# Kernel tuning notes

Measured on AMD Instinct MI355X. Metric: run time of the kernel, lower is better.

The kernel has to match this reference:

```python
import jax, jax.numpy as jnp
import numpy as np
from jax import lax

DN = ('NCHW', 'OIHW', 'NCHW')

def conv(x, w, b, stride, pad):
    y = lax.conv_general_dilated(x, w, (stride, stride), [(pad, pad), (pad, pad)], dimension_numbers=DN)
    return y + b[None, :, None, None]

def setup_inputs() -> dict:
    key = jax.random.key(0)
    ks = jax.random.split(key, 16)
    s = 0.05
    inp = {
        'condition': jax.random.normal(ks[0], (16, 1, 256, 256), jnp.float32),
        'w1': jax.random.normal(ks[1], (64, 1, 4, 4), jnp.float32) * s,
        'b1': jnp.zeros((64,), jnp.float32),
        'w2': jax.random.normal(ks[2], (128, 64, 4, 4), jnp.float32) * s,
        'b2': jnp.zeros((128,), jnp.float32),
        'w3': jax.random.normal(ks[3], (128, 128, 3, 3), jnp.float32) * s,
        'b3': jnp.zeros((128,), jnp.float32),
        'r1w1': jax.random.normal(ks[4], (32, 128, 3, 3), jnp.float32) * s,
        'r1b1': jnp.zeros((32,), jnp.float32),
        'r1w2': jax.random.normal(ks[5], (128, 32, 1, 1), jnp.float32) * s,
        'r1b2': jnp.zeros((128,), jnp.float32),
        'r2w1': jax.random.normal(ks[6], (32, 128, 3, 3), jnp.float32) * s,
        'r2b1': jnp.zeros((32,), jnp.float32),
        'r2w2': jax.random.normal(ks[7], (128, 32, 1, 1), jnp.float32) * s,
        'r2b2': jnp.zeros((128,), jnp.float32),
        'wpre': jax.random.normal(ks[8], (4, 128, 1, 1), jnp.float32) * s,
        'bpre': jnp.zeros((4,), jnp.float32),
        'codebook': jax.random.normal(ks[9], (2048, 4), jnp.float32),
    }
    return inp

def reference(condition, w1, b1, w2, b2, w3, b3, r1w1, r1b1, r1w2, r1b2,
              r2w1, r2b1, r2w2, r2b2, wpre, bpre, codebook):
    # --- conv encoder (VQ-VAE standard) ---
    h = jax.nn.relu(conv(condition, w1, b1, 2, 1))   # [B,64,128,128]
    h = jax.nn.relu(conv(h, w2, b2, 2, 1))           # [B,128,64,64]
    h = conv(h, w3, b3, 1, 1)                        # [B,128,64,64]
    # residual stack: 2 blocks of relu->3x3->relu->1x1, residual add
    for wa, ba, wb, bb in ((r1w1, r1b1, r1w2, r1b2), (r2w1, r2b1, r2w2, r2b2)):
        t = conv(jax.nn.relu(h), wa, ba, 1, 1)
        t = conv(jax.nn.relu(t), wb, bb, 1, 0)
        h = h + t
    h = jax.nn.relu(h)
    z = conv(h, wpre, bpre, 1, 0)                    # [B,4,64,64]
    # --- cosine-distance vector quantization ---
    B, D, H, W = z.shape
    zf = jnp.transpose(z, (0, 2, 3, 1)).reshape(-1, D)          # [BHW, D]
    zn = zf / (jnp.linalg.norm(zf, axis=-1, keepdims=True) + 1e-12)
    en = codebook / (jnp.linalg.norm(codebook, axis=-1, keepdims=True) + 1e-12)
    sim = jnp.einsum('nd,kd->nk', zn, en)                       # cosine similarity
    idx = jnp.argmax(sim, axis=-1)                              # nearest code
    q = codebook[idx].reshape(B, H, W, D)
    c = jnp.transpose(q, (0, 3, 1, 2))                          # [B,4,64,64]
    return c
```

## Files before the change

### kernel.cpp

```cpp
#include <hip/hip_runtime.h>
#include <math.h>


typedef short v8s __attribute__((ext_vector_type(8)));
typedef float v4f __attribute__((ext_vector_type(4)));

#define B_OFF 4194304
#define A_OFF 12582912
#define ENCB_F 1048576
#define ZB_F 2097152
#define W2_S 0
#define W3_S 393216
#define WR1_S 835584
#define WR2_S 946176
#define WP1_S 1056768
#define WP2_S 1069056

__device__ inline void limb3(float v, unsigned short& h, unsigned short& m,
                             unsigned short& l) {
    unsigned ub = __float_as_uint(v);
    unsigned hb = ub & 0xffff0000u;
    float r1 = v - __uint_as_float(hb);
    unsigned mb = __float_as_uint(r1) & 0xffff0000u;
    float r2 = r1 - __uint_as_float(mb);
    unsigned lb = __float_as_uint(r2) & 0xffff0000u;
    h = (unsigned short)(hb >> 16);
    m = (unsigned short)(mb >> 16);
    l = (unsigned short)(lb >> 16);
}

struct CfgConv2 {
    static constexpr int NC = 8, NT = 4, OC = 128;
    static constexpr bool RELU_IN = false, RELU_OUT = true;
    __device__ static void tap(int c, int t, int& ry, int& rx) {
        int py = (c >> 2) & 1, px = (c >> 1) & 1;
        ry = (t >> 1) - py; rx = (t & 1) - px;
    }
    __device__ static bool gaddr(int n, int oy, int r, int X, int icp, int c,
                                 int& g0, int& g1) {
        int py = (c >> 2) & 1, px = (c >> 1) & 1;
        int y2 = oy + r - 1;
        if (y2 < 0 || y2 >= 64) return false;
        int pi = (c & 1) * 16 + icp;
        g0 = (((n * 4 + py * 2 + px) * 64 + y2) * 32 + pi) * 128 + X;
        g1 = g0 + 64;
        return true;
    }
    __device__ static int widx(int c, int t, int oc, int ic) {
        int py = (c >> 2) & 1, px = (c >> 1) & 1, half = c & 1;
        int dy = 2 * (t >> 1) + (1 - py), dx = 2 * (t & 1) + (1 - px);
        return ((oc * 64 + half * 32 + ic) * 4 + dy) * 4 + dx;
    }
};
struct CfgConv3 {
    static constexpr int NC = 4, NT = 9, OC = 128;
    static constexpr bool RELU_IN = false, RELU_OUT = false;
    __device__ static void tap(int c, int t, int& ry, int& rx) {
        ry = t / 3 - 1; rx = t % 3 - 1;
    }
    __device__ static bool gaddr(int n, int oy, int r, int X, int icp, int c,
                                 int& g0, int& g1) {
        int Yg = oy + r - 1;
        if (Yg < 0 || Yg >= 64) return false;
        int pi = c * 16 + icp;
        g0 = ((n * 64 + Yg) * 64 + pi) * 128 + X;
        g1 = g0 + 64;
        return true;
    }
    __device__ static int widx(int c, int t, int oc, int ic) {
        return ((oc * 128 + c * 32 + ic) * 3 + t / 3) * 3 + t % 3;
    }
};
struct CfgRes {
    static constexpr int NC = 4, NT = 9, OC = 32;
    __device__ static int widx(int c, int t, int oc, int ic) {
        return ((oc * 128 + c * 32 + ic) * 3 + t / 3) * 3 + t % 3;
    }
};
struct Cfg1x1 {
    static constexpr int NC = 1, NT = 1, OC = 128;
    __device__ static int widx(int c, int t, int oc, int ic) {
        return oc * 32 + ic;
    }
};

template <typename C>
__device__ inline void repack_one(const float* __restrict__ w,
                                  short* __restrict__ dst, int idx) {
    int s  = idx & 31;
    int oc = (idx >> 5) % C::OC;
    int ct = idx / (32 * C::OC);
    int c = ct / C::NT, t = ct % C::NT;
    float val = w[C::widx(c, t, oc, s)];
    unsigned short h, m, l;
    limb3(val, h, m, l);
    constexpr int NTILE = C::OC / 16;
    int nt = oc >> 4, o = oc & 15, q = s >> 3, j = s & 7;
    int fr = ((q * 16 + o) << 3) + j;
    dst[(((ct * 3 + 0) * NTILE + nt) << 9) + fr] = (short)h;
    dst[(((ct * 3 + 1) * NTILE + nt) << 9) + fr] = (short)m;
    dst[(((ct * 3 + 2) * NTILE + nt) << 9) + fr] = (short)l;
}

__global__ __launch_bounds__(256) void repack_all_k(
    const float* __restrict__ w2, const float* __restrict__ w3,
    const float* __restrict__ r1, const float* __restrict__ r2,
    const float* __restrict__ p1, const float* __restrict__ p2,
    const float* __restrict__ cb, short* __restrict__ base,
    float* __restrict__ encb)
{
    int idx = blockIdx.x * 256 + threadIdx.x;
    if (idx < 131072) { repack_one<CfgConv2>(w2, base + W2_S, idx); return; }
    idx -= 131072;
    if (idx < 147456) { repack_one<CfgConv3>(w3, base + W3_S, idx); return; }
    idx -= 147456;
    if (idx < 36864)  { repack_one<CfgRes>(r1, base + WR1_S, idx); return; }
    idx -= 36864;
    if (idx < 36864)  { repack_one<CfgRes>(r2, base + WR2_S, idx); return; }
    idx -= 36864;
    if (idx < 4096)   { repack_one<Cfg1x1>(p1, base + WP1_S, idx); return; }
    idx -= 4096;
    if (idx < 4096)   { repack_one<Cfg1x1>(p2, base + WP2_S, idx); return; }
    idx -= 4096;
    if (idx < 8192) {
        int k = idx >> 2, d = idx & 3;
        float c0 = cb[k * 4 + 0], c1 = cb[k * 4 + 1];
        float c2 = cb[k * 4 + 2], c3 = cb[k * 4 + 3];
        float nrm = sqrtf(c0 * c0 + c1 * c1 + c2 * c2 + c3 * c3) + 1e-12f;
        encb[k * 4 + d] = cb[k * 4 + d] / nrm;
    }
}

template <typename C>
__global__ __launch_bounds__(256, 3) void mfma_conv(
    const float* __restrict__ in, const short* __restrict__ repw,
    const float* __restrict__ bias, float* __restrict__ out, int n0)
{
    constexpr int APLANE = 3 * 66 * 32;
    constexpr int NTILE  = C::OC / 16;
    __shared__ __align__(16) short lA[3 * APLANE];

    int tid = threadIdx.x;
    int lane = tid & 63, wv = tid >> 6;
    int n_img = blockIdx.x >> 6, oy = blockIdx.x & 63;

    for (int idx = tid; idx < 3 * 3 * 2 * 16; idx += 256) {
        int plane = idx / 96;
        int rem = idx % 96;
        int rr = rem / 32;
        int hc = (rem / 16) & 1;
        int d = idx & 15;
        ((unsigned*)lA)[plane * 3168 + (rr * 66 + hc * 65) * 16 + d] = 0;
    }

    v4f acc[4][2] = {};
    int nbase = wv * 2;
    int Xq = tid & 15, icp = tid >> 4, quad = lane >> 4;

    float pv[24];
    auto issue_loads = [&](int c) {
#pragma unroll
        for (int it = 0; it < 12; it++) {
            int r = it >> 2, xg = it & 3;
            int X = xg * 16 + Xq;
            int g0, g1;
            float v0 = 0.f, v1 = 0.f;
            if (C::gaddr(n_img, oy, r, X, icp, c, g0, g1)) {
                v0 = in[g0];
                v1 = in[g1];
            }
            pv[2 * it] = v0; pv[2 * it + 1] = v1;
        }
    };
    auto load_bf = [&](int c, int t, v8s (&dst)[2][3]) {
#pragma unroll
        for (int nt = 0; nt < 2; nt++)
#pragma unroll
            for (int L = 0; L < 3; L++)
                dst[nt][L] = *(const v8s*)(repw +
                    ((((c * C::NT + t) * 3 + L) * NTILE + (nbase + nt)) << 9) +
                    (lane << 3));
    };

    issue_loads(0);

    for (int c = 0; c < C::NC; c++) {
        __syncthreads();
#pragma unroll
        for (int it = 0; it < 12; it++) {
            int r = it >> 2, xg = it & 3;
            int X = xg * 16 + Xq;
            float v0 = pv[2 * it], v1 = pv[2 * it + 1];
            if constexpr (C::RELU_IN) { v0 = fmaxf(v0, 0.f); v1 = fmaxf(v1, 0.f); }
            unsigned short h0, m0, l0, h1, m1, l1;
            limb3(v0, h0, m0, l0);
            limb3(v1, h1, m1, l1);
            int cell = r * 66 + X + 1;
            int f = (cell + (cell >> 2)) & 3;
            int phys = (icp & 3) + 4 * (((icp >> 2) + f) & 3);
            unsigned* pa = (unsigned*)lA + cell * 16 + phys;
            pa[0]        = (unsigned)h0 | ((unsigned)h1 << 16);
            pa[3168]     = (unsigned)m0 | ((unsigned)m1 << 16);
            pa[2 * 3168] = (unsigned)l0 | ((unsigned)l1 << 16);
        }
        __syncthreads();
        if (c + 1 < C::NC) issue_loads(c + 1);

        v8s bf[2][2][3];
        load_bf(c, 0, bf[0]);
#pragma unroll
        for (int t = 0; t < C::NT; t++) {
            constexpr int NTT = C::NT;
            if (t + 1 < NTT) load_bf(c, t + 1, bf[(t + 1) & 1]);
            int ry, rx;
            C::tap(c, t, ry, rx);
#pragma unroll
            for (int mt = 0; mt < 4; mt++) {
                int x = mt * 16 + (lane & 15);
                int cell = (ry + 1) * 66 + (x + rx + 1);
                int f = (cell + (cell >> 2)) & 3;
                int aa = cell * 32 + (((quad + f) & 3) << 3);
                v8s ah = *(const v8s*)&lA[aa];
                v8s am = *(const v8s*)&lA[APLANE + aa];
                v8s al = *(const v8s*)&lA[2 * APLANE + aa];
#pragma unroll
                for (int nt = 0; nt < 2; nt++) {
                    v4f a0 = acc[mt][nt];
                    a0 = __builtin_amdgcn_mfma_f32_16x16x32_bf16(ah, bf[t & 1][nt][0], a0, 0, 0, 0);
                    a0 = __builtin_amdgcn_mfma_f32_16x16x32_bf16(ah, bf[t & 1][nt][1], a0, 0, 0, 0);
                    a0 = __builtin_amdgcn_mfma_f32_16x16x32_bf16(am, bf[t & 1][nt][0], a0, 0, 0, 0);
                    a0 = __builtin_amdgcn_mfma_f32_16x16x32_bf16(am, bf[t & 1][nt][1], a0, 0, 0, 0);
                    a0 = __builtin_amdgcn_mfma_f32_16x16x32_bf16(ah, bf[t & 1][nt][2], a0, 0, 0, 0);
                    a0 = __builtin_amdgcn_mfma_f32_16x16x32_bf16(al, bf[t & 1][nt][0], a0, 0, 0, 0);
                    acc[mt][nt] = a0;
                }
            }
        }
    }
#pragma unroll
    for (int mt = 0; mt < 4; mt++) {
        int x0 = mt * 16 + quad * 4;
#pragma unroll
        for (int nt = 0; nt < 2; nt++) {
            int oc = (nbase + nt) * 16 + (lane & 15);
            float bv = bias[oc];
            float v0 = acc[mt][nt][0] + bv;
            float v1 = acc[mt][nt][1] + bv;
            float v2 = acc[mt][nt][2] + bv;
            float v3 = acc[mt][nt][3] + bv;
            if constexpr (C::RELU_OUT) {
                v0 = fmaxf(v0, 0.f); v1 = fmaxf(v1, 0.f);
                v2 = fmaxf(v2, 0.f); v3 = fmaxf(v3, 0.f);
            }
            float4 o = make_float4(v0, v1, v2, v3);
            int off = (((n0 + n_img) * 64 + oy) * 64 + (oc >> 1)) * 128 +
                      (oc & 1) * 64 + x0;
            *(float4*)&out[off] = o;
        }
    }
}

__global__ __launch_bounds__(256) void mfma_res(
    const float* __restrict__ in, const short* __restrict__ repw,
    const float* __restrict__ b1, const short* __restrict__ repp,
    const float* __restrict__ b2, float* __restrict__ out)
{
    constexpr int PLANE_D = 4 * 66 * 16;
    constexpr int PLANE_S = 2 * PLANE_D;
    __shared__ __align__(16) short lA[3 * PLANE_S];

    int tid = threadIdx.x;
    int lane = tid & 63, wv = tid >> 6;
    int n_img = blockIdx.x >> 5;
    int oy0 = (blockIdx.x & 31) << 1;
    int jrow = wv >> 1, xh = wv & 1;

    for (int idx = tid; idx < 3 * 4 * 2 * 16; idx += 256) {
        int plane = idx / 128;
        int rem = idx % 128;
        int rr = rem / 32;
        int hc = (rem >> 4) & 1;
        int d = idx & 15;
        ((unsigned*)lA)[plane * PLANE_D + (rr * 66 + hc * 65) * 16 + d] = 0;
    }

    v4f acc[2][2] = {};
    int Xq = tid & 15, icp = tid >> 4, quad = lane >> 4;

    float pv[32];
    auto issue_loads = [&](int c) {
#pragma unroll
        for (int it = 0; it < 16; it++) {
            int r = it >> 2, xg = it & 3;
            int X = xg * 16 + Xq;
            int Yg = oy0 + r - 1;
            float v0 = 0.f, v1 = 0.f;
            if (Yg >= 0 && Yg < 64) {
                int g = ((n_img * 64 + Yg) * 64 + (c * 16 + icp)) * 128 + X;
                v0 = in[g];
                v1 = in[g + 64];
            }
            pv[2 * it] = v0; pv[2 * it + 1] = v1;
        }
    };

    issue_loads(0);

    for (int c = 0; c < 4; c++) {
        __syncthreads();
#pragma unroll
        for (int it = 0; it < 16; it++) {
            int r = it >> 2, xg = it & 3;
            int X = xg * 16 + Xq;
            float v0 = fmaxf(pv[2 * it], 0.f);
            float v1 = fmaxf(pv[2 * it + 1], 0.f);
            unsigned short h0, m0, l0, h1, m1, l1;
            limb3(v0, h0, m0, l0);
            limb3(v1, h1, m1, l1);
            int cell = r * 66 + X + 1;
            int f = (cell + (cell >> 2)) & 3;
            int phys = (icp & 3) + 4 * (((icp >> 2) + f) & 3);
            unsigned* pa = (unsigned*)lA + cell * 16 + phys;
            pa[0]           = (unsigned)h0 | ((unsigned)h1 << 16);
            pa[PLANE_D]     = (unsigned)m0 | ((unsigned)m1 << 16);
            pa[2 * PLANE_D] = (unsigned)l0 | ((unsigned)l1 << 16);
        }
        __syncthreads();
        if (c + 1 < 4) issue_loads(c + 1);

        v8s bf[2][2][3];
        auto load_bf = [&](int t, v8s (&dst)[2][3]) {
#pragma unroll
            for (int nt = 0; nt < 2; nt++)
#pragma unroll
                for (int L = 0; L < 3; L++)
                    dst[nt][L] = *(const v8s*)(repw +
                        ((((c * 9 + t) * 3 + L) * 2 + nt) << 9) + (lane << 3));
        };
        load_bf(0, bf[0]);
#pragma unroll
        for (int t = 0; t < 9; t++) {
            if (t + 1 < 9) load_bf(t + 1, bf[(t + 1) & 1]);
            int ry = t / 3 - 1, rx = t % 3 - 1;
#pragma unroll
            for (int mti = 0; mti < 2; mti++) {
                int x = (xh * 2 + mti) * 16 + (lane & 15);
                int cell = (jrow + ry + 1) * 66 + (x + rx + 1);
                int f = (cell + (cell >> 2)) & 3;
                int aa = cell * 32 + (((quad + f) & 3) << 3);
                v8s ah = *(const v8s*)&lA[aa];
                v8s am = *(const v8s*)&lA[PLANE_S + aa];
                v8s al = *(const v8s*)&lA[2 * PLANE_S + aa];
#pragma unroll
                for (int nt = 0; nt < 2; nt++) {
                    v4f a0 = acc[mti][nt];
                    a0 = __builtin_amdgcn_mfma_f32_16x16x32_bf16(ah, bf[t & 1][nt][0], a0, 0, 0, 0);
                    a0 = __builtin_amdgcn_mfma_f32_16x16x32_bf16(ah, bf[t & 1][nt][1], a0, 0, 0, 0);
                    a0 = __builtin_amdgcn_mfma_f32_16x16x32_bf16(am, bf[t & 1][nt][0], a0, 0, 0, 0);
                    a0 = __builtin_amdgcn_mfma_f32_16x16x32_bf16(am, bf[t & 1][nt][1], a0, 0, 0, 0);
                    a0 = __builtin_amdgcn_mfma_f32_16x16x32_bf16(ah, bf[t & 1][nt][2], a0, 0, 0, 0);
                    a0 = __builtin_amdgcn_mfma_f32_16x16x32_bf16(al, bf[t & 1][nt][0], a0, 0, 0, 0);
                    acc[mti][nt] = a0;
                }
            }
        }
    }

    __syncthreads();
#pragma unroll
    for (int mti = 0; mti < 2; mti++) {
#pragma unroll
        for (int nt = 0; nt < 2; nt++) {
            int ic = nt * 16 + (lane & 15);
            int icp2 = ic >> 1, hilo = ic & 1;
            float bv = b1[ic];
#pragma unroll
            for (int r = 0; r < 4; r++) {
                int x = (xh * 2 + mti) * 16 + quad * 4 + r;
                float v = fmaxf(acc[mti][nt][r] + bv, 0.f);
                unsigned short h, m, l;
                limb3(v, h, m, l);
                int f = (x + (x >> 2)) & 3;
                int phys = (icp2 & 3) + 4 * (((icp2 >> 2) + f) & 3);
                int sa = x * 32 + phys * 2 + hilo;
                lA[jrow * 6144 + sa]        = (short)h;
                lA[jrow * 6144 + 2048 + sa] = (short)m;
                lA[jrow * 6144 + 4096 + sa] = (short)l;
            }
        }
    }
    __syncthreads();

#pragma unroll
    for (int j = 0; j < 2; j++) {
        v4f a2[8] = {};
        int x = wv * 16 + (lane & 15);
        int f = (x + (x >> 2)) & 3;
        int aa = x * 32 + (((quad + f) & 3) << 3);
        v8s ah = *(const v8s*)&lA[j * 6144 + aa];
        v8s am = *(const v8s*)&lA[j * 6144 + 2048 + aa];
        v8s al = *(const v8s*)&lA[j * 6144 + 4096 + aa];
#pragma unroll
        for (int nt = 0; nt < 8; nt++) {
            v8s bh = *(const v8s*)(repp + ((0 * 8 + nt) << 9) + (lane << 3));
            v8s bm = *(const v8s*)(repp + ((1 * 8 + nt) << 9) + (lane << 3));
            v8s bl = *(const v8s*)(repp + ((2 * 8 + nt) << 9) + (lane << 3));
            v4f a0 = a2[nt];
            a0 = __builtin_amdgcn_mfma_f32_16x16x32_bf16(ah, bh, a0, 0, 0, 0);
            a0 = __builtin_amdgcn_mfma_f32_16x16x32_bf16(ah, bm, a0, 0, 0, 0);
            a0 = __builtin_amdgcn_mfma_f32_16x16x32_bf16(am, bh, a0, 0, 0, 0);
            a0 = __builtin_amdgcn_mfma_f32_16x16x32_bf16(am, bm, a0, 0, 0, 0);
            a0 = __builtin_amdgcn_mfma_f32_16x16x32_bf16(ah, bl, a0, 0, 0, 0);
            a0 = __builtin_amdgcn_mfma_f32_16x16x32_bf16(al, bh, a0, 0, 0, 0);
            a2[nt] = a0;
        }
#pragma unroll
        for (int nt = 0; nt < 8; nt++) {
            int oc = nt * 16 + (lane & 15);
            int x0 = wv * 16 + quad * 4;
            int off = ((n_img * 64 + (oy0 + j)) * 64 + (oc >> 1)) * 128 +
                      (oc & 1) * 64 + x0;
            float4 hv = *(const float4*)&in[off];
            float bv = b2[oc];
            float4 o = make_float4(hv.x + a2[nt][0] + bv, hv.y + a2[nt][1] + bv,
                                   hv.z + a2[nt][2] + bv, hv.w + a2[nt][3] + bv);
            *(float4*)&out[off] = o;
        }
    }
}

__global__ __launch_bounds__(256) void mfma_res_vq(
    const float* __restrict__ in, const short* __restrict__ repw,
    const float* __restrict__ b1, const short* __restrict__ repp,
    const float* __restrict__ b2, const float* __restrict__ wpre,
    const float* __restrict__ bpre, float* __restrict__ zbuf)
{
    constexpr int PLANE_D = 4 * 66 * 16;
    constexpr int PLANE_S = 2 * PLANE_D;
    __shared__ __align__(16) short lA[3 * PLANE_S];

    int tid = threadIdx.x;
    int lane = tid & 63, wv = tid >> 6;
    int n_img = blockIdx.x >> 5;
    int oy0 = (blockIdx.x & 31) << 1;
    int jrow = wv >> 1, xh = wv & 1;

    for (int idx = tid; idx < 3 * 4 * 2 * 16; idx += 256) {
        int plane = idx / 128;
        int rem = idx % 128;
        int rr = rem / 32;
        int hc = (rem >> 4) & 1;
        int d = idx & 15;
        ((unsigned*)lA)[plane * PLANE_D + (rr * 66 + hc * 65) * 16 + d] = 0;
    }

    v4f acc[2][2] = {};
    int Xq = tid & 15, icp = tid >> 4, quad = lane >> 4;

    float pv[32];
    auto issue_loads = [&](int c) {
#pragma unroll
        for (int it = 0; it < 16; it++) {
            int r = it >> 2, xg = it & 3;
            int X = xg * 16 + Xq;
            int Yg = oy0 + r - 1;
            float v0 = 0.f, v1 = 0.f;
            if (Yg >= 0 && Yg < 64) {
                int g = ((n_img * 64 + Yg) * 64 + (c * 16 + icp)) * 128 + X;
                v0 = in[g];
                v1 = in[g + 64];
            }
            pv[2 * it] = v0; pv[2 * it + 1] = v1;
        }
    };

    issue_loads(0);

    for (int c = 0; c < 4; c++) {
        __syncthreads();
#pragma unroll
        for (int it = 0; it < 16; it++) {
            int r = it >> 2, xg = it & 3;
            int X = xg * 16 + Xq;
            float v0 = fmaxf(pv[2 * it], 0.f);
            float v1 = fmaxf(pv[2 * it + 1], 0.f);
            unsigned short h0, m0, l0, h1, m1, l1;
            limb3(v0, h0, m0, l0);
            limb3(v1, h1, m1, l1);
            int cell = r * 66 + X + 1;
            int f = (cell + (cell >> 2)) & 3;
            int phys = (icp & 3) + 4 * (((icp >> 2) + f) & 3);
            unsigned* pa = (unsigned*)lA + cell * 16 + phys;
            pa[0]           = (unsigned)h0 | ((unsigned)h1 << 16);
            pa[PLANE_D]     = (unsigned)m0 | ((unsigned)m1 << 16);
            pa[2 * PLANE_D] = (unsigned)l0 | ((unsigned)l1 << 16);
        }
        __syncthreads();
        if (c + 1 < 4) issue_loads(c + 1);

        v8s bf[2][2][3];
        auto load_bf = [&](int t, v8s (&dst)[2][3]) {
#pragma unroll
            for (int nt = 0; nt < 2; nt++)
#pragma unroll
                for (int L = 0; L < 3; L++)
                    dst[nt][L] = *(const v8s*)(repw +
                        ((((c * 9 + t) * 3 + L) * 2 + nt) << 9) + (lane << 3));
        };
        load_bf(0, bf[0]);
#pragma unroll
        for (int t = 0; t < 9; t++) {
            if (t + 1 < 9) load_bf(t + 1, bf[(t + 1) & 1]);
            int ry = t / 3 - 1, rx = t % 3 - 1;
#pragma unroll
            for (int mti = 0; mti < 2; mti++) {
                int x = (xh * 2 + mti) * 16 + (lane & 15);
                int cell = (jrow + ry + 1) * 66 + (x + rx + 1);
                int f = (cell + (cell >> 2)) & 3;
                int aa = cell * 32 + (((quad + f) & 3) << 3);
                v8s ah = *(const v8s*)&lA[aa];
                v8s am = *(const v8s*)&lA[PLANE_S + aa];
                v8s al = *(const v8s*)&lA[2 * PLANE_S + aa];
#pragma unroll
                for (int nt = 0; nt < 2; nt++) {
                    v4f a0 = acc[mti][nt];
                    a0 = __builtin_amdgcn_mfma_f32_16x16x32_bf16(ah, bf[t & 1][nt][0], a0, 0, 0, 0);
                    a0 = __builtin_amdgcn_mfma_f32_16x16x32_bf16(ah, bf[t & 1][nt][1], a0, 0, 0, 0);
                    a0 = __builtin_amdgcn_mfma_f32_16x16x32_bf16(am, bf[t & 1][nt][0], a0, 0, 0, 0);
                    a0 = __builtin_amdgcn_mfma_f32_16x16x32_bf16(am, bf[t & 1][nt][1], a0, 0, 0, 0);
                    a0 = __builtin_amdgcn_mfma_f32_16x16x32_bf16(ah, bf[t & 1][nt][2], a0, 0, 0, 0);
                    a0 = __builtin_amdgcn_mfma_f32_16x16x32_bf16(al, bf[t & 1][nt][0], a0, 0, 0, 0);
                    acc[mti][nt] = a0;
                }
            }
        }
    }

    __syncthreads();
#pragma unroll
    for (int mti = 0; mti < 2; mti++) {
#pragma unroll
        for (int nt = 0; nt < 2; nt++) {
            int ic = nt * 16 + (lane & 15);
            int icp2 = ic >> 1, hilo = ic & 1;
            float bv = b1[ic];
#pragma unroll
            for (int r = 0; r < 4; r++) {
                int x = (xh * 2 + mti) * 16 + quad * 4 + r;
                float v = fmaxf(acc[mti][nt][r] + bv, 0.f);
                unsigned short h, m, l;
                limb3(v, h, m, l);
                int f = (x + (x >> 2)) & 3;
                int phys = (icp2 & 3) + 4 * (((icp2 >> 2) + f) & 3);
                int sa = x * 32 + phys * 2 + hilo;
                lA[jrow * 6144 + sa]        = (short)h;
                lA[jrow * 6144 + 2048 + sa] = (short)m;
                lA[jrow * 6144 + 4096 + sa] = (short)l;
            }
        }
    }
    __syncthreads();

    float wp[8][4];
#pragma unroll
    for (int nt = 0; nt < 8; nt++)
#pragma unroll
        for (int d = 0; d < 4; d++)
            wp[nt][d] = wpre[d * 128 + nt * 16 + (lane & 15)];

#pragma unroll
    for (int j = 0; j < 2; j++) {
        v4f a2[8] = {};
        int x = wv * 16 + (lane & 15);
        int f = (x + (x >> 2)) & 3;
        int aa = x * 32 + (((quad + f) & 3) << 3);
        v8s ah = *(const v8s*)&lA[j * 6144 + aa];
        v8s am = *(const v8s*)&lA[j * 6144 + 2048 + aa];
        v8s al = *(const v8s*)&lA[j * 6144 + 4096 + aa];
#pragma unroll
        for (int nt = 0; nt < 8; nt++) {
            v8s bh = *(const v8s*)(repp + ((0 * 8 + nt) << 9) + (lane << 3));
            v8s bm = *(const v8s*)(repp + ((1 * 8 + nt) << 9) + (lane << 3));
            v8s bl = *(const v8s*)(repp + ((2 * 8 + nt) << 9) + (lane << 3));
            v4f a0 = a2[nt];
            a0 = __builtin_amdgcn_mfma_f32_16x16x32_bf16(ah, bh, a0, 0, 0, 0);
            a0 = __builtin_amdgcn_mfma_f32_16x16x32_bf16(ah, bm, a0, 0, 0, 0);
            a0 = __builtin_amdgcn_mfma_f32_16x16x32_bf16(am, bh, a0, 0, 0, 0);
            a0 = __builtin_amdgcn_mfma_f32_16x16x32_bf16(am, bm, a0, 0, 0, 0);
            a0 = __builtin_amdgcn_mfma_f32_16x16x32_bf16(ah, bl, a0, 0, 0, 0);
            a0 = __builtin_amdgcn_mfma_f32_16x16x32_bf16(al, bh, a0, 0, 0, 0);
            a2[nt] = a0;
        }
        float z[4][4];
#pragma unroll
        for (int r = 0; r < 4; r++)
#pragma unroll
            for (int d = 0; d < 4; d++) z[r][d] = 0.f;
#pragma unroll
        for (int nt = 0; nt < 8; nt++) {
            int oc = nt * 16 + (lane & 15);
            int x0 = wv * 16 + quad * 4;
            int off = ((n_img * 64 + (oy0 + j)) * 64 + (oc >> 1)) * 128 +
                      (oc & 1) * 64 + x0;
            float4 hv = *(const float4*)&in[off];
            float bv = b2[oc];
            float o0 = fmaxf(hv.x + a2[nt][0] + bv, 0.f);
            float o1 = fmaxf(hv.y + a2[nt][1] + bv, 0.f);
            float o2 = fmaxf(hv.z + a2[nt][2] + bv, 0.f);
            float o3 = fmaxf(hv.w + a2[nt][3] + bv, 0.f);
#pragma unroll
            for (int d = 0; d < 4; d++) {
                z[0][d] = fmaf(o0, wp[nt][d], z[0][d]);
                z[1][d] = fmaf(o1, wp[nt][d], z[1][d]);
                z[2][d] = fmaf(o2, wp[nt][d], z[2][d]);
                z[3][d] = fmaf(o3, wp[nt][d], z[3][d]);
            }
        }
#pragma unroll
        for (int mask = 1; mask < 16; mask <<= 1)
#pragma unroll
            for (int r = 0; r < 4; r++)
#pragma unroll
                for (int d = 0; d < 4; d++)
                    z[r][d] += __shfl_xor(z[r][d], mask);
        int l15 = lane & 15;
#pragma unroll
        for (int r = 0; r < 4; r++)
#pragma unroll
            for (int d = 0; d < 4; d++)
                if (l15 == r * 4 + d)
                    zbuf[(((n_img * 64 + oy0 + j) * 64) + wv * 16 + quad * 4 + r) * 4 + d]
                        = z[r][d] + bpre[d];
    }
}

__global__ __launch_bounds__(256) void scan_vq(
    const float* __restrict__ zbuf, const float* __restrict__ encb,
    const float* __restrict__ cb, float* __restrict__ out)
{
    __shared__ __align__(16) float en[2048 * 4];
    __shared__ float cwS[4][64];
    __shared__ int   cwI[4][64];
    for (int i = threadIdx.x; i < 2048; i += 256)
        ((float4*)en)[i] = ((const float4*)encb)[i];
    __syncthreads();

    int lane = threadIdx.x & 63, w = threadIdx.x >> 6;
    int gpos = blockIdx.x * 64 + lane;
    float4 zv = ((const float4*)zbuf)[gpos];

    int kb = w * 512;
    float b0 = -1e30f, b1 = -1e30f, b2 = -1e30f, b3 = -1e30f;
    int i0 = kb, i1 = kb + 1, i2 = kb + 2, i3 = kb + 3;
    for (int i = 0; i < 512; i += 4) {
        float4 e0 = ((const float4*)en)[kb + i];
        float4 e1 = ((const float4*)en)[kb + i + 1];
        float4 e2 = ((const float4*)en)[kb + i + 2];
        float4 e3 = ((const float4*)en)[kb + i + 3];
        float s0 = zv.x * e0.x + zv.y * e0.y + zv.z * e0.z + zv.w * e0.w;
        float s1 = zv.x * e1.x + zv.y * e1.y + zv.z * e1.z + zv.w * e1.w;
        float s2 = zv.x * e2.x + zv.y * e2.y + zv.z * e2.z + zv.w * e2.w;
        float s3 = zv.x * e3.x + zv.y * e3.y + zv.z * e3.z + zv.w * e3.w;
        if (s0 > b0) { b0 = s0; i0 = kb + i; }
        if (s1 > b1) { b1 = s1; i1 = kb + i + 1; }
        if (s2 > b2) { b2 = s2; i2 = kb + i + 2; }
        if (s3 > b3) { b3 = s3; i3 = kb + i + 3; }
    }
    float best = b0; int bidx = i0;
    if (b1 > best || (b1 == best && i1 < bidx)) { best = b1; bidx = i1; }
    if (b2 > best || (b2 == best && i2 < bidx)) { best = b2; bidx = i2; }
    if (b3 > best || (b3 == best && i3 < bidx)) { best = b3; bidx = i3; }
    cwS[w][lane] = best;
    cwI[w][lane] = bidx;
    __syncthreads();
    if (w == 0) {
#pragma unroll
        for (int ww = 1; ww < 4; ww++) {
            float ob = cwS[ww][lane];
            int   oi = cwI[ww][lane];
            if (ob > best || (ob == best && oi < bidx)) { best = ob; bidx = oi; }
        }
        int n = gpos >> 12, pos = gpos & 4095;
#pragma unroll
        for (int d = 0; d < 4; d++)
            out[(n * 4 + d) * 4096 + pos] = cb[bidx * 4 + d];
    }
}

__global__ __launch_bounds__(256) void conv1_k(
    const float* __restrict__ x, const float* __restrict__ w,
    const float* __restrict__ b, float* __restrict__ out)
{
    int tid = blockIdx.x * 256 + threadIdx.x;
    int n   = tid >> 14;
    int rem = tid & 16383;
    int oy  = rem >> 7;
    int ox  = rem & 127;
    int iy0 = oy * 2 - 1, ix0 = ox * 2 - 1;
    const float* xb = x + n * 65536;
    float v[16];
#pragma unroll
    for (int ky = 0; ky < 4; ky++) {
#pragma unroll
        for (int kx = 0; kx < 4; kx++) {
            int iy = iy0 + ky, ix = ix0 + kx;
            bool ok = (iy >= 0) & (iy < 256) & (ix >= 0) & (ix < 256);
            v[ky * 4 + kx] = ok ? xb[iy * 256 + ix] : 0.f;
        }
    }
    int py = oy & 1, y2 = oy >> 1, px = ox & 1, x2 = ox >> 1;
    int obase = (((n * 4 + py * 2 + px) * 64 + y2) * 32) * 128 + x2;
    for (int oc = 0; oc < 64; oc++) {
        float acc = b[oc];
        const float* wp = w + oc * 16;
#pragma unroll
        for (int k = 0; k < 16; k++) acc = fmaf(v[k], wp[k], acc);
        out[obase + (oc >> 1) * 128 + (oc & 1) * 64] = fmaxf(acc, 0.f);
    }
}

extern "C" void kernel_launch(void* const* d_in, const int* in_sizes, int n_in,
                              void* d_out, int out_size, void* d_ws, size_t ws_size,
                              hipStream_t stream)
{
    const float* x    = (const float*)d_in[0];
    const float* w1   = (const float*)d_in[1];
    const float* b1   = (const float*)d_in[2];
    const float* w2   = (const float*)d_in[3];
    const float* b2   = (const float*)d_in[4];
    const float* w3   = (const float*)d_in[5];
    const float* b3   = (const float*)d_in[6];
    const float* r1w1 = (const float*)d_in[7];
    const float* r1b1 = (const float*)d_in[8];
    const float* r1w2 = (const float*)d_in[9];
    const float* r1b2 = (const float*)d_in[10];
    const float* r2w1 = (const float*)d_in[11];
    const float* r2b1 = (const float*)d_in[12];
    const float* r2w2 = (const float*)d_in[13];
    const float* r2b2 = (const float*)d_in[14];
    const float* wpre = (const float*)d_in[15];
    const float* bpre = (const float*)d_in[16];
    const float* cb   = (const float*)d_in[17];
    float* out = (float*)d_out;

    float* ws   = (float*)d_ws;
    short* wsS  = (short*)d_ws;
    float* encb = ws + ENCB_F;
    float* zbuf = ws + ZB_F;
    float* B = ws + B_OFF;
    float* A = ws + A_OFF;

    repack_all_k<<<1440, 256, 0, stream>>>(w2, w3, r1w1, r2w1, r1w2, r2w2,
                                           cb, wsS, encb);

    conv1_k<<<512, 256, 0, stream>>>(x,               w1, b1, A);
    mfma_conv<CfgConv2><<<512, 256, 0, stream>>>(A, wsS + W2_S, b2, B, 0);
    conv1_k<<<512, 256, 0, stream>>>(x + 8 * 65536,   w1, b1, A);
    mfma_conv<CfgConv2><<<512, 256, 0, stream>>>(A, wsS + W2_S, b2, B, 8);

    mfma_conv<CfgConv3><<<1024, 256, 0, stream>>>(B, wsS + W3_S, b3, A, 0);

    mfma_res<<<512, 256, 0, stream>>>(A, wsS + WR1_S, r1b1, wsS + WP1_S, r1b2, B);
    mfma_res_vq<<<512, 256, 0, stream>>>(B, wsS + WR2_S, r2b1, wsS + WP2_S,
                                         r2b2, wpre, bpre, zbuf);
    scan_vq<<<1024, 256, 0, stream>>>(zbuf, encb, cb, out);
}
```

Before: 426.3 us.

## Split residual-block tiles in half along x to double grid size

Both residual kernels now give each block a 2-row by 32-column output tile instead of 2 rows by 64 columns, with a halo read from global memory, and launch 1024 blocks instead of 512. Each wave handles a single 16-pixel M-tile and one output row, which cuts accumulator and staging registers, shrinks LDS per block, and adds a launch_bounds occupancy hint of 4 blocks. The aim is more blocks in flight and higher occupancy to hide latency. The cost is redundant halo loads and limb-splitting work, plus each block reloading the same weights for half as much output.

```diff
diff --git a/kernel.cpp b/kernel.cpp
--- a/kernel.cpp
+++ b/kernel.cpp
@@ -260,43 +260,37 @@
     }
 }
 
-__global__ __launch_bounds__(256) void mfma_res(
+__global__ __launch_bounds__(256, 4) void mfma_res(
     const float* __restrict__ in, const short* __restrict__ repw,
     const float* __restrict__ b1, const short* __restrict__ repp,
     const float* __restrict__ b2, float* __restrict__ out)
 {
-    constexpr int PLANE_D = 4 * 66 * 16;
+    constexpr int PLANE_D = 4 * 36 * 16;
     constexpr int PLANE_S = 2 * PLANE_D;
     __shared__ __align__(16) short lA[3 * PLANE_S];
 
     int tid = threadIdx.x;
     int lane = tid & 63, wv = tid >> 6;
-    int n_img = blockIdx.x >> 5;
-    int oy0 = (blockIdx.x & 31) << 1;
-    int jrow = wv >> 1, xh = wv & 1;
-
-    for (int idx = tid; idx < 3 * 4 * 2 * 16; idx += 256) {
-        int plane = idx / 128;
-        int rem = idx % 128;
-        int rr = rem / 32;
-        int hc = (rem >> 4) & 1;
-        int d = idx & 15;
-        ((unsigned*)lA)[plane * PLANE_D + (rr * 66 + hc * 65) * 16 + d] = 0;
-    }
-
-    v4f acc[2][2] = {};
+    int n_img = blockIdx.x >> 6;
+    int sub = blockIdx.x & 63;
+    int oy0 = (sub >> 1) << 1;
+    int xh2 = sub & 1;
+    int jrow = wv >> 1, xhw = wv & 1;
+
+    v4f acc[2] = {};
     int Xq = tid & 15, icp = tid >> 4, quad = lane >> 4;
 
-    float pv[32];
+    float pv[24];
     auto issue_loads = [&](int c) {
 #pragma unroll
-        for (int it = 0; it < 16; it++) {
-            int r = it >> 2, xg = it & 3;
-            int X = xg * 16 + Xq;
+        for (int it = 0; it < 12; it++) {
+            int r = it / 3, xg = it % 3;
+            int lx = xg * 16 + Xq;
+            int Xg = xh2 * 32 + lx - 1;
             int Yg = oy0 + r - 1;
             float v0 = 0.f, v1 = 0.f;
-            if (Yg >= 0 && Yg < 64) {
-                int g = ((n_img * 64 + Yg) * 64 + (c * 16 + icp)) * 128 + X;
+            if (Yg >= 0 && Yg < 64 && Xg >= 0 && Xg < 64) {
+                int g = ((n_img * 64 + Yg) * 64 + (c * 16 + icp)) * 128 + Xg;
                 v0 = in[g];
                 v1 = in[g + 64];
             }
@@ -309,21 +303,23 @@
     for (int c = 0; c < 4; c++) {
         __syncthreads();
 #pragma unroll
-        for (int it = 0; it < 16; it++) {
-            int r = it >> 2, xg = it & 3;
-            int X = xg * 16 + Xq;
+        for (int it = 0; it < 12; it++) {
+            int r = it / 3, xg = it % 3;
+            int lx = xg * 16 + Xq;
             float v0 = fmaxf(pv[2 * it], 0.f);
             float v1 = fmaxf(pv[2 * it + 1], 0.f);
             unsigned short h0, m0, l0, h1, m1, l1;
             limb3(v0, h0, m0, l0);
             limb3(v1, h1, m1, l1);
-            int cell = r * 66 + X + 1;
-            int f = (cell + (cell >> 2)) & 3;
-            int phys = (icp & 3) + 4 * (((icp >> 2) + f) & 3);
-            unsigned* pa = (unsigned*)lA + cell * 16 + phys;
-            pa[0]           = (unsigned)h0 | ((unsigned)h1 << 16);
-            pa[PLANE_D]     = (unsigned)m0 | ((unsigned)m1 << 16);
-            pa[2 * PLANE_D] = (unsigned)l0 | ((unsigned)l1 << 16);
+            if (lx < 34) {
+                int cell = r * 36 + lx;
+                int f = (cell + (cell >> 2)) & 3;
+                int phys = (icp & 3) + 4 * (((icp >> 2) + f) & 3);
+                unsigned* pa = (unsigned*)lA + cell * 16 + phys;
+                pa[0]           = (unsigned)h0 | ((unsigned)h1 << 16);
+                pa[PLANE_D]     = (unsigned)m0 | ((unsigned)m1 << 16);
+                pa[2 * PLANE_D] = (unsigned)l0 | ((unsigned)l1 << 16);
+            }
         }
         __syncthreads();
         if (c + 1 < 4) issue_loads(c + 1);
@@ -342,64 +338,57 @@
         for (int t = 0; t < 9; t++) {
             if (t + 1 < 9) load_bf(t + 1, bf[(t + 1) & 1]);
             int ry = t / 3 - 1, rx = t % 3 - 1;
-#pragma unroll
-            for (int mti = 0; mti < 2; mti++) {
-                int x = (xh * 2 + mti) * 16 + (lane & 15);
-                int cell = (jrow + ry + 1) * 66 + (x + rx + 1);
-                int f = (cell + (cell >> 2)) & 3;
-                int aa = cell * 32 + (((quad + f) & 3) << 3);
-                v8s ah = *(const v8s*)&lA[aa];
-                v8s am = *(const v8s*)&lA[PLANE_S + aa];
-                v8s al = *(const v8s*)&lA[2 * PLANE_S + aa];
-#pragma unroll
-                for (int nt = 0; nt < 2; nt++) {
-                    v4f a0 = acc[mti][nt];
-                    a0 = __builtin_amdgcn_mfma_f32_16x16x32_bf16(ah, bf[t & 1][nt][0], a0, 0, 0, 0);
-                    a0 = __builtin_amdgcn_mfma_f32_16x16x32_bf16(ah, bf[t & 1][nt][1], a0, 0, 0, 0);
-                    a0 = __builtin_amdgcn_mfma_f32_16x16x32_bf16(am, bf[t & 1][nt][0], a0, 0, 0, 0);
-                    a0 = __builtin_amdgcn_mfma_f32_16x16x32_bf16(am, bf[t & 1][nt][1], a0, 0, 0, 0);
-                    a0 = __builtin_amdgcn_mfma_f32_16x16x32_bf16(ah, bf[t & 1][nt][2], a0, 0, 0, 0);
-                    a0 = __builtin_amdgcn_mfma_f32_16x16x32_bf16(al, bf[t & 1][nt][0], a0, 0, 0, 0);
-                    acc[mti][nt] = a0;
-                }
+            int lxw = xhw * 16 + (lane & 15);
+            int cell = (jrow + ry + 1) * 36 + (lxw + rx + 1);
+            int f = (cell + (cell >> 2)) & 3;
+            int aa = cell * 32 + (((quad + f) & 3) << 3);
+            v8s ah = *(const v8s*)&lA[aa];
+            v8s am = *(const v8s*)&lA[PLANE_S + aa];
+            v8s al = *(const v8s*)&lA[2 * PLANE_S + aa];
+#pragma unroll
+            for (int nt = 0; nt < 2; nt++) {
+                v4f a0 = acc[nt];
+                a0 = __builtin_amdgcn_mfma_f32_16x16x32_bf16(ah, bf[t & 1][nt][0], a0, 0, 0, 0);
+                a0 = __builtin_amdgcn_mfma_f32_16x16x32_bf16(ah, bf[t & 1][nt][1], a0, 0, 0, 0);
+                a0 = __builtin_amdgcn_mfma_f32_16x16x32_bf16(am, bf[t & 1][nt][0], a0, 0, 0, 0);
+                a0 = __builtin_amdgcn_mfma_f32_16x16x32_bf16(am, bf[t & 1][nt][1], a0, 0, 0, 0);
+                a0 = __builtin_amdgcn_mfma_f32_16x16x32_bf16(ah, bf[t & 1][nt][2], a0, 0, 0, 0);
+                a0 = __builtin_amdgcn_mfma_f32_16x16x32_bf16(al, bf[t & 1][nt][0], a0, 0, 0, 0);
+                acc[nt] = a0;
             }
         }
     }
 
     __syncthreads();
 #pragma unroll
-    for (int mti = 0; mti < 2; mti++) {
-#pragma unroll
-        for (int nt = 0; nt < 2; nt++) {
-            int ic = nt * 16 + (lane & 15);
-            int icp2 = ic >> 1, hilo = ic & 1;
-            float bv = b1[ic];
-#pragma unroll
-            for (int r = 0; r < 4; r++) {
-                int x = (xh * 2 + mti) * 16 + quad * 4 + r;
-                float v = fmaxf(acc[mti][nt][r] + bv, 0.f);
-                unsigned short h, m, l;
-                limb3(v, h, m, l);
-                int f = (x + (x >> 2)) & 3;
-                int phys = (icp2 & 3) + 4 * (((icp2 >> 2) + f) & 3);
-                int sa = x * 32 + phys * 2 + hilo;
-                lA[jrow * 6144 + sa]        = (short)h;
-                lA[jrow * 6144 + 2048 + sa] = (short)m;
-                lA[jrow * 6144 + 4096 + sa] = (short)l;
-            }
+    for (int nt = 0; nt < 2; nt++) {
+        int ic = nt * 16 + (lane & 15);
+        int icp2 = ic >> 1, hilo = ic & 1;
+        float bv = b1[ic];
+#pragma unroll
+        for (int r = 0; r < 4; r++) {
+            int xr = xhw * 16 + quad * 4 + r;
+            float v = fmaxf(acc[nt][r] + bv, 0.f);
+            unsigned short h, m, l;
+            limb3(v, h, m, l);
+            int f = (xr + (xr >> 2)) & 3;
+            int phys = (icp2 & 3) + 4 * (((icp2 >> 2) + f) & 3);
+            int sa = xr * 32 + phys * 2 + hilo;
+            lA[jrow * 1024 + sa]        = (short)h;
+            lA[2048 + jrow * 1024 + sa] = (short)m;
+            lA[4096 + jrow * 1024 + sa] = (short)l;
         }
     }
     __syncthreads();
 
-#pragma unroll
-    for (int j = 0; j < 2; j++) {
-        v4f a2[8] = {};
-        int x = wv * 16 + (lane & 15);
-        int f = (x + (x >> 2)) & 3;
-        int aa = x * 32 + (((quad + f) & 3) << 3);
-        v8s ah = *(const v8s*)&lA[j * 6144 + aa];
-        v8s am = *(const v8s*)&lA[j * 6144 + 2048 + aa];
-        v8s al = *(const v8s*)&lA[j * 6144 + 4096 + aa];
+    v4f a2[8] = {};
+    {
+        int xr = xhw * 16 + (lane & 15);
+        int f = (xr + (xr >> 2)) & 3;
+        int aa = xr * 32 + (((quad + f) & 3) << 3);
+        v8s ah = *(const v8s*)&lA[jrow * 1024 + aa];
+        v8s am = *(const v8s*)&lA[2048 + jrow * 1024 + aa];
+        v8s al = *(const v8s*)&lA[4096 + jrow * 1024 + aa];
 #pragma unroll
         for (int nt = 0; nt < 8; nt++) {
             v8s bh = *(const v8s*)(repp + ((0 * 8 + nt) << 9) + (lane << 3));
@@ -414,59 +403,53 @@
             a0 = __builtin_amdgcn_mfma_f32_16x16x32_bf16(al, bh, a0, 0, 0, 0);
             a2[nt] = a0;
         }
-#pragma unroll
-        for (int nt = 0; nt < 8; nt++) {
-            int oc = nt * 16 + (lane & 15);
-            int x0 = wv * 16 + quad * 4;
-            int off = ((n_img * 64 + (oy0 + j)) * 64 + (oc >> 1)) * 128 +
-                      (oc & 1) * 64 + x0;
-            float4 hv = *(const float4*)&in[off];
-            float bv = b2[oc];
-            float4 o = make_float4(hv.x + a2[nt][0] + bv, hv.y + a2[nt][1] + bv,
-                                   hv.z + a2[nt][2] + bv, hv.w + a2[nt][3] + bv);
-            *(float4*)&out[off] = o;
-        }
-    }
-}
-
-__global__ __launch_bounds__(256) void mfma_res_vq(
+    }
+#pragma unroll
+    for (int nt = 0; nt < 8; nt++) {
+        int oc = nt * 16 + (lane & 15);
+        int x0 = xh2 * 32 + xhw * 16 + quad * 4;
+        int off = ((n_img * 64 + (oy0 + jrow)) * 64 + (oc >> 1)) * 128 +
+                  (oc & 1) * 64 + x0;
+        float4 hv = *(const float4*)&in[off];
+        float bv = b2[oc];
+        float4 o = make_float4(hv.x + a2[nt][0] + bv, hv.y + a2[nt][1] + bv,
+                               hv.z + a2[nt][2] + bv, hv.w + a2[nt][3] + bv);
+        *(float4*)&out[off] = o;
+    }
+}
+
+__global__ __launch_bounds__(256, 4) void mfma_res_vq(
     const float* __restrict__ in, const short* __restrict__ repw,
     const float* __restrict__ b1, const short* __restrict__ repp,
     const float* __restrict__ b2, const float* __restrict__ wpre,
     const float* __restrict__ bpre, float* __restrict__ zbuf)
 {
-    constexpr int PLANE_D = 4 * 66 * 16;
+    constexpr int PLANE_D = 4 * 36 * 16;
     constexpr int PLANE_S = 2 * PLANE_D;
     __shared__ __align__(16) short lA[3 * PLANE_S];
 
     int tid = threadIdx.x;
     int lane = tid & 63, wv = tid >> 6;
-    int n_img = blockIdx.x >> 5;
-    int oy0 = (blockIdx.x & 31) << 1;
-    int jrow = wv >> 1, xh = wv & 1;
-
-    for (int idx = tid; idx < 3 * 4 * 2 * 16; idx += 256) {
-        int plane = idx / 128;
-        int rem = idx % 128;
-        int rr = rem / 32;
-        int hc = (rem >> 4) & 1;
-        int d = idx & 15;
-        ((unsigned*)lA)[plane * PLANE_D + (rr * 66 + hc * 65) * 16 + d] = 0;
-    }
-
-    v4f acc[2][2] = {};
+    int n_img = blockIdx.x >> 6;
+    int sub = blockIdx.x & 63;
+    int oy0 = (sub >> 1) << 1;
+    int xh2 = sub & 1;
+    int jrow = wv >> 1, xhw = wv & 1;
+
+    v4f acc[2] = {};
     int Xq = tid & 15, icp = tid >> 4, quad = lane >> 4;
 
-    float pv[32];
+    float pv[24];
     auto issue_loads = [&](int c) {
 #pragma unroll
-        for (int it = 0; it < 16; it++) {
-            int r = it >> 2, xg = it & 3;
-            int X = xg * 16 + Xq;
+        for (int it = 0; it < 12; it++) {
+            int r = it / 3, xg = it % 3;
+            int lx = xg * 16 + Xq;
+            int Xg = xh2 * 32 + lx - 1;
             int Yg = oy0 + r - 1;
             float v0 = 0.f, v1 = 0.f;
-            if (Yg >= 0 && Yg < 64) {
-                int g = ((n_img * 64 + Yg) * 64 + (c * 16 + icp)) * 128 + X;
+            if (Yg >= 0 && Yg < 64 && Xg >= 0 && Xg < 64) {
+                int g = ((n_img * 64 + Yg) * 64 + (c * 16 + icp)) * 128 + Xg;
                 v0 = in[g];
                 v1 = in[g + 64];
             }
@@ -479,21 +462,23 @@
     for (int c = 0; c < 4; c++) {
         __syncthreads();
 #pragma unroll
-        for (int it = 0; it < 16; it++) {
-            int r = it >> 2, xg = it & 3;
-            int X = xg * 16 + Xq;
+        for (int it = 0; it < 12; it++) {
+            int r = it / 3, xg = it % 3;
+            int lx = xg * 16 + Xq;
             float v0 = fmaxf(pv[2 * it], 0.f);
             float v1 = fmaxf(pv[2 * it + 1], 0.f);
             unsigned short h0, m0, l0, h1, m1, l1;
             limb3(v0, h0, m0, l0);
             limb3(v1, h1, m1, l1);
-            int cell = r * 66 + X + 1;
-            int f = (cell + (cell >> 2)) & 3;
-            int phys = (icp & 3) + 4 * (((icp >> 2) + f) & 3);
-            unsigned* pa = (unsigned*)lA + cell * 16 + phys;
-            pa[0]           = (unsigned)h0 | ((unsigned)h1 << 16);
-            pa[PLANE_D]     = (unsigned)m0 | ((unsigned)m1 << 16);
-            pa[2 * PLANE_D] = (unsigned)l0 | ((unsigned)l1 << 16);
+            if (lx < 34) {
+                int cell = r * 36 + lx;
+                int f = (cell + (cell >> 2)) & 3;
+                int phys = (icp & 3) + 4 * (((icp >> 2) + f) & 3);
+                unsigned* pa = (unsigned*)lA + cell * 16 + phys;
+                pa[0]           = (unsigned)h0 | ((unsigned)h1 << 16);
+                pa[PLANE_D]     = (unsigned)m0 | ((unsigned)m1 << 16);
+                pa[2 * PLANE_D] = (unsigned)l0 | ((unsigned)l1 << 16);
+            }
         }
         __syncthreads();
         if (c + 1 < 4) issue_loads(c + 1);
@@ -512,51 +497,45 @@
         for (int t = 0; t < 9; t++) {
             if (t + 1 < 9) load_bf(t + 1, bf[(t + 1) & 1]);
             int ry = t / 3 - 1, rx = t % 3 - 1;
-#pragma unroll
-            for (int mti = 0; mti < 2; mti++) {
-                int x = (xh * 2 + mti) * 16 + (lane & 15);
-                int cell = (jrow + ry + 1) * 66 + (x + rx + 1);
-                int f = (cell + (cell >> 2)) & 3;
-                int aa = cell * 32 + (((quad + f) & 3) << 3);
-                v8s ah = *(const v8s*)&lA[aa];
-                v8s am = *(const v8s*)&lA[PLANE_S + aa];
-                v8s al = *(const v8s*)&lA[2 * PLANE_S + aa];
-#pragma unroll
-                for (int nt = 0; nt < 2; nt++) {
-                    v4f a0 = acc[mti][nt];
-                    a0 = __builtin_amdgcn_mfma_f32_16x16x32_bf16(ah, bf[t & 1][nt][0], a0, 0, 0, 0);
-                    a0 = __builtin_amdgcn_mfma_f32_16x16x32_bf16(ah, bf[t & 1][nt][1], a0, 0, 0, 0);
-                    a0 = __builtin_amdgcn_mfma_f32_16x16x32_bf16(am, bf[t & 1][nt][0], a0, 0, 0, 0);
-                    a0 = __builtin_amdgcn_mfma_f32_16x16x32_bf16(am, bf[t & 1][nt][1], a0, 0, 0, 0);
-                    a0 = __builtin_amdgcn_mfma_f32_16x16x32_bf16(ah, bf[t & 1][nt][2], a0, 0, 0, 0);
-                    a0 = __builtin_amdgcn_mfma_f32_16x16x32_bf16(al, bf[t & 1][nt][0], a0, 0, 0, 0);
-                    acc[mti][nt] = a0;
-                }
+            int lxw = xhw * 16 + (lane & 15);
+            int cell = (jrow + ry + 1) * 36 + (lxw + rx + 1);
+            int f = (cell + (cell >> 2)) & 3;
+            int aa = cell * 32 + (((quad + f) & 3) << 3);
+            v8s ah = *(const v8s*)&lA[aa];
+            v8s am = *(const v8s*)&lA[PLANE_S + aa];
+            v8s al = *(const v8s*)&lA[2 * PLANE_S + aa];
+#pragma unroll
+            for (int nt = 0; nt < 2; nt++) {
+                v4f a0 = acc[nt];
+                a0 = __builtin_amdgcn_mfma_f32_16x16x32_bf16(ah, bf[t & 1][nt][0], a0, 0, 0, 0);
+                a0 = __builtin_amdgcn_mfma_f32_16x16x32_bf16(ah, bf[t & 1][nt][1], a0, 0, 0, 0);
+                a0 = __builtin_amdgcn_mfma_f32_16x16x32_bf16(am, bf[t & 1][nt][0], a0, 0, 0, 0);
+                a0 = __builtin_amdgcn_mfma_f32_16x16x32_bf16(am, bf[t & 1][nt][1], a0, 0, 0, 0);
+                a0 = __builtin_amdgcn_mfma_f32_16x16x32_bf16(ah, bf[t & 1][nt][2], a0, 0, 0, 0);
+                a0 = __builtin_amdgcn_mfma_f32_16x16x32_bf16(al, bf[t & 1][nt][0], a0, 0, 0, 0);
+                acc[nt] = a0;
             }
         }
     }
 
     __syncthreads();
 #pragma unroll
-    for (int mti = 0; mti < 2; mti++) {
-#pragma unroll
-        for (int nt = 0; nt < 2; nt++) {
-            int ic = nt * 16 + (lane & 15);
-            int icp2 = ic >> 1, hilo = ic & 1;
-            float bv = b1[ic];
-#pragma unroll
-            for (int r = 0; r < 4; r++) {
-                int x = (xh * 2 + mti) * 16 + quad * 4 + r;
-                float v = fmaxf(acc[mti][nt][r] + bv, 0.f);
-                unsigned short h, m, l;
-                limb3(v, h, m, l);
-                int f = (x + (x >> 2)) & 3;
-                int phys = (icp2 & 3) + 4 * (((icp2 >> 2) + f) & 3);
-                int sa = x * 32 + phys * 2 + hilo;
-                lA[jrow * 6144 + sa]        = (short)h;
-                lA[jrow * 6144 + 2048 + sa] = (short)m;
-                lA[jrow * 6144 + 4096 + sa] = (short)l;
-            }
+    for (int nt = 0; nt < 2; nt++) {
+        int ic = nt * 16 + (lane & 15);
+        int icp2 = ic >> 1, hilo = ic & 1;
+        float bv = b1[ic];
+#pragma unroll
+        for (int r = 0; r < 4; r++) {
+            int xr = xhw * 16 + quad * 4 + r;
+            float v = fmaxf(acc[nt][r] + bv, 0.f);
+            unsigned short h, m, l;
+            limb3(v, h, m, l);
+            int f = (xr + (xr >> 2)) & 3;
+            int phys = (icp2 & 3) + 4 * (((icp2 >> 2) + f) & 3);
+            int sa = xr * 32 + phys * 2 + hilo;
+            lA[jrow * 1024 + sa]        = (short)h;
+            lA[2048 + jrow * 1024 + sa] = (short)m;
+            lA[4096 + jrow * 1024 + sa] = (short)l;
         }
     }
     __syncthreads();
@@ -568,15 +547,14 @@
         for (int d = 0; d < 4; d++)
             wp[nt][d] = wpre[d * 128 + nt * 16 + (lane & 15)];
 
-#pragma unroll
-    for (int j = 0; j < 2; j++) {
-        v4f a2[8] = {};
-        int x = wv * 16 + (lane & 15);
-        int f = (x + (x >> 2)) & 3;
-        int aa = x * 32 + (((quad + f) & 3) << 3);
-        v8s ah = *(const v8s*)&lA[j * 6144 + aa];
-        v8s am = *(const v8s*)&lA[j * 6144 + 2048 + aa];
-        v8s al = *(const v8s*)&lA[j * 6144 + 4096 + aa];
+    v4f a2[8] = {};
+    {
+        int xr = xhw * 16 + (lane & 15);
+        int f = (xr + (xr >> 2)) & 3;
+        int aa = xr * 32 + (((quad + f) & 3) << 3);
+        v8s ah = *(const v8s*)&lA[jrow * 1024 + aa];
+        v8s am = *(const v8s*)&lA[2048 + jrow * 1024 + aa];
+        v8s al = *(const v8s*)&lA[4096 + jrow * 1024 + aa];
 #pragma unroll
         for (int nt = 0; nt < 8; nt++) {
             v8s bh = *(const v8s*)(repp + ((0 * 8 + nt) << 9) + (lane << 3));
@@ -591,46 +569,50 @@
             a0 = __builtin_amdgcn_mfma_f32_16x16x32_bf16(al, bh, a0, 0, 0, 0);
             a2[nt] = a0;
         }
-        float z[4][4];
+    }
+    float z[4][4];
+#pragma unroll
+    for (int r = 0; r < 4; r++)
+#pragma unroll
+        for (int d = 0; d < 4; d++) z[r][d] = 0.f;
+#pragma unroll
+    for (int nt = 0; nt < 8; nt++) {
+        int oc = nt * 16 + (lane & 15);
+        int x0 = xh2 * 32 + xhw * 16 + quad * 4;
+        int off = ((n_img * 64 + (oy0 + jrow)) * 64 + (oc >> 1)) * 128 +
+                  (oc & 1) * 64 + x0;
+        float4 hv = *(const float4*)&in[off];
+        float bv = b2[oc];
+        float o0 = fmaxf(hv.x + a2[nt][0] + bv, 0.f);
+        float o1 = fmaxf(hv.y + a2[nt][1] + bv, 0.f);
+        float o2 = fmaxf(hv.z + a2[nt][2] + bv, 0.f);
+        float o3 = fmaxf(hv.w + a2[nt][3] + bv, 0.f);
+#pragma unroll
+        for (int d = 0; d < 4; d++) {
+            z[0][d] = fmaf(o0, wp[nt][d], z[0][d]);
+            z[1][d] = fmaf(o1, wp[nt][d], z[1][d]);
+            z[2][d] = fmaf(o2, wp[nt][d], z[2][d]);
+            z[3][d] = fmaf(o3, wp[nt][d], z[3][d]);
+        }
+    }
+#pragma unroll
+    for (int mask = 1; mask < 16; mask <<= 1)
 #pragma unroll
         for (int r = 0; r < 4; r++)
 #pragma unroll
-            for (int d = 0; d < 4; d++) z[r][d] = 0.f;
-#pragma unroll
-        for (int nt = 0; nt < 8; nt++) {
-            int oc = nt * 16 + (lane & 15);
-            int x0 = wv * 16 + quad * 4;
-            int off = ((n_img * 64 + (oy0 + j)) * 64 + (oc >> 1)) * 128 +
-                      (oc & 1) * 64 + x0;
-            float4 hv = *(const float4*)&in[off];
-            float bv = b2[oc];
-            float o0 = fmaxf(hv.x + a2[nt][0] + bv, 0.f);
-            float o1 = fmaxf(hv.y + a2[nt][1] + bv, 0.f);
-            float o2 = fmaxf(hv.z + a2[nt][2] + bv, 0.f);
-            float o3 = fmaxf(hv.w + a2[nt][3] + bv, 0.f);
-#pragma unroll
-            for (int d = 0; d < 4; d++) {
-                z[0][d] = fmaf(o0, wp[nt][d], z[0][d]);
-                z[1][d] = fmaf(o1, wp[nt][d], z[1][d]);
-                z[2][d] = fmaf(o2, wp[nt][d], z[2][d]);
-                z[3][d] = fmaf(o3, wp[nt][d], z[3][d]);
-            }
-        }
-#pragma unroll
-        for (int mask = 1; mask < 16; mask <<= 1)
-#pragma unroll
-            for (int r = 0; r < 4; r++)
-#pragma unroll
-                for (int d = 0; d < 4; d++)
-                    z[r][d] += __shfl_xor(z[r][d], mask);
+            for (int d = 0; d < 4; d++)
+                z[r][d] += __shfl_xor(z[r][d], mask);
+    {
         int l15 = lane & 15;
 #pragma unroll
         for (int r = 0; r < 4; r++)
 #pragma unroll
             for (int d = 0; d < 4; d++)
-                if (l15 == r * 4 + d)
-                    zbuf[(((n_img * 64 + oy0 + j) * 64) + wv * 16 + quad * 4 + r) * 4 + d]
+                if (l15 == r * 4 + d) {
+                    int xg0 = xh2 * 32 + xhw * 16 + quad * 4 + r;
+                    zbuf[(((n_img * 64 + oy0 + jrow) * 64) + xg0) * 4 + d]
                         = z[r][d] + bpre[d];
+                }
     }
 }
 
@@ -760,8 +742,8 @@
 
     mfma_conv<CfgConv3><<<1024, 256, 0, stream>>>(B, wsS + W3_S, b3, A, 0);
 
-    mfma_res<<<512, 256, 0, stream>>>(A, wsS + WR1_S, r1b1, wsS + WP1_S, r1b2, B);
-    mfma_res_vq<<<512, 256, 0, stream>>>(B, wsS + WR2_S, r2b1, wsS + WP2_S,
-                                         r2b2, wpre, bpre, zbuf);
+    mfma_res<<<1024, 256, 0, stream>>>(A, wsS + WR1_S, r1b1, wsS + WP1_S, r1b2, B);
+    mfma_res_vq<<<1024, 256, 0, stream>>>(B, wsS + WR2_S, r2b1, wsS + WP2_S,
+                                          r2b2, wpre, bpre, zbuf);
     scan_vq<<<1024, 256, 0, stream>>>(zbuf, encb, cb, out);
 }
```

Measured after the change: 451.6 us. 1.06x slower.
